# Kernel optimization log

Hardware: AMD Instinct MI355X
Metric: run time of the kernel (lower is better)

The kernel has to match this reference:

```python
import jax, jax.numpy as jnp
import numpy as np
from jax.ops import segment_sum

N_NODES = 50000


def gcn_conv(x, src, dst, W, b, n_nodes):
    # PyG GCNConv with default add_self_loops=True, normalize=True.
    # deg includes self-loops (weight 1 each).
    deg = segment_sum(jnp.ones_like(dst, dtype=x.dtype), dst, num_segments=n_nodes) + 1.0
    dinv = jax.lax.rsqrt(deg)  # [N]
    h = x @ W                  # [N, out]
    # messages over real edges: norm[src]*norm[dst]*h[src]
    msg = h[src] * (dinv[src] * dinv[dst])[:, None]   # [E, out]
    agg = segment_sum(msg, dst, num_segments=n_nodes)  # [N, out]
    # self-loop contribution: dinv[i]^2 * h[i]
    agg = agg + h * (dinv * dinv)[:, None]
    return agg + b


def setup_inputs() -> dict:
    key = jax.random.key(0)
    k1, k2, k3, k4 = jax.random.split(key, 4)
    N, E, d_in, d_hid, d_out = N_NODES, 800000, 128, 128, 64
    x = jax.random.normal(k1, (N, d_in), dtype=jnp.float32)
    edge_index = jax.random.randint(k2, (2, E), 0, N, dtype=jnp.int64)
    W1 = jax.random.normal(k3, (d_in, d_hid), dtype=jnp.float32) / np.sqrt(d_in)
    b1 = jnp.zeros((d_hid,), dtype=jnp.float32)
    W2 = jax.random.normal(k4, (d_hid, d_out), dtype=jnp.float32) / np.sqrt(d_hid)
    b2 = jnp.zeros((d_out,), dtype=jnp.float32)
    return {"x": x, "edge_index": edge_index, "W1": W1, "b1": b1, "W2": W2, "b2": b2}


def reference(x, edge_index, W1, b1, W2, b2):
    src, dst = edge_index[0], edge_index[1]
    h = gcn_conv(x, src, dst, W1, b1, N_NODES)
    h = jax.nn.relu(h)
    out = gcn_conv(h, src, dst, W2, b2, N_NODES)
    return out
```

## Files before the change

### kernel.cpp

```cpp
#include <hip/hip_runtime.h>
#include <hip/hip_bf16.h>


#define ELL_CAP 64
#define NPART 8

typedef __attribute__((ext_vector_type(8))) short short8;
typedef __attribute__((ext_vector_type(4))) float f32x4;

static __device__ __forceinline__ unsigned short f2bf(float f) {
    unsigned int u = __float_as_uint(f);
    u = (u + 0x7fff + ((u >> 16) & 1)) >> 16;
    return (unsigned short)u;
}
static __device__ __forceinline__ float2 bfunpack(unsigned int u) {
    return make_float2(__uint_as_float(u << 16),
                       __uint_as_float(u & 0xffff0000u));
}


__global__ void zero_cnt(int* __restrict__ cnt, int n) {
    int i = blockIdx.x * blockDim.x + threadIdx.x;
    if (i < n) cnt[i] = 0;
}

__global__ __launch_bounds__(256) void build_ell_part(
    const int* __restrict__ src, const int* __restrict__ dst,
    int* __restrict__ cnt, int* __restrict__ ell, int E, int partSize)
{
    const int part   = blockIdx.x & (NPART - 1);
    const int chunk  = blockIdx.x >> 3;
    const int nchunk = gridDim.x >> 3;
    const int lo = part * partSize, hi = lo + partSize;
    const int per = (E + nchunk - 1) / nchunk;
    const int e1 = min((chunk + 1) * per, E);
    for (int e = chunk * per + threadIdx.x; e < e1; e += 256) {
        int d = dst[e];
        if (d >= lo && d < hi) {
            int pos = atomicAdd(&cnt[d], 1);
            if (pos < ELL_CAP) ell[(size_t)d * ELL_CAP + pos] = src[e];
        }
    }
}

__global__ void convert_weights(const float* __restrict__ W1, const float* __restrict__ W2,
                                short* __restrict__ w1t, short* __restrict__ w2t)
{
    int i = blockIdx.x * blockDim.x + threadIdx.x;
    if (i < 128 * 128) {
        int k = i >> 7, nn = i & 127;
        w1t[nn * 128 + k] = (short)f2bf(W1[i]);
    } else if (i < 128 * 128 + 128 * 64) {
        int j = i - 128 * 128;
        int k = j >> 6, nn = j & 63;
        w2t[nn * 128 + k] = (short)f2bf(W2[j]);
    }
}


template<int NC, bool AF32>
__global__ __launch_bounds__(256) void gemm_mfma(
    const void* __restrict__ Av, const short* __restrict__ Bt,
    const int* __restrict__ cnt, unsigned short* __restrict__ Cb, int n)
{
    __shared__ short Bs[NC][136];
    const int tid = threadIdx.x;

    #pragma unroll
    for (int i = 0; i < NC / 16; ++i) {
        int idx = tid + i * 256;
        int nrow = idx >> 4;
        int kcol = (idx & 15) * 8;
        *(short8*)&Bs[nrow][kcol] = *(const short8*)(Bt + nrow * 128 + kcol);
    }
    __syncthreads();

    const int wave = tid >> 6, lane = tid & 63;
    const int row0 = blockIdx.x * 64 + wave * 16;
    if (row0 >= n) return;
    const int quad = lane >> 4, l16 = lane & 15;

    short8 af[4];
    if (AF32) {
        const float* arow = (const float*)Av + (size_t)(row0 + l16) * 128 + quad * 8;
        #pragma unroll
        for (int kk = 0; kk < 4; ++kk) {
            float4 u = *(const float4*)(arow + kk * 32);
            float4 v = *(const float4*)(arow + kk * 32 + 4);
            short8 f;
            f[0] = (short)f2bf(u.x); f[1] = (short)f2bf(u.y);
            f[2] = (short)f2bf(u.z); f[3] = (short)f2bf(u.w);
            f[4] = (short)f2bf(v.x); f[5] = (short)f2bf(v.y);
            f[6] = (short)f2bf(v.z); f[7] = (short)f2bf(v.w);
            af[kk] = f;
        }
    } else {
        const short* arow = (const short*)Av + (size_t)(row0 + l16) * 128 + quad * 8;
        #pragma unroll
        for (int kk = 0; kk < 4; ++kk)
            af[kk] = *(const short8*)(arow + kk * 32);
    }

    float dv[4];
    #pragma unroll
    for (int r = 0; r < 4; ++r)
        dv[r] = rsqrtf((float)cnt[row0 + quad * 4 + r] + 1.0f);

    #pragma unroll
    for (int t = 0; t < NC / 16; ++t) {
        f32x4 acc = {0.f, 0.f, 0.f, 0.f};
        #pragma unroll
        for (int kk = 0; kk < 4; ++kk) {
            short8 bfr = *(const short8*)&Bs[t * 16 + l16][kk * 32 + quad * 8];
            acc = __builtin_amdgcn_mfma_f32_16x16x32_bf16(af[kk], bfr, acc, 0, 0, 0);
        }
        #pragma unroll
        for (int r = 0; r < 4; ++r) {
            int gr = row0 + quad * 4 + r;
            Cb[(size_t)gr * NC + t * 16 + l16] = f2bf(acc[r] * dv[r]);
        }
    }
}


__global__ __launch_bounds__(256) void aggregate_l1(
    const unsigned int* __restrict__ hp, const int* __restrict__ ell,
    const int* __restrict__ cnt, const float* __restrict__ bias,
    unsigned int* __restrict__ z1b, int n)
{
    int node = blockIdx.x * 4 + (threadIdx.x >> 6);
    if (node >= n) return;
    int lane = threadIdx.x & 63;
    int deg = cnt[node];
    float d = rsqrtf((float)deg + 1.0f);
    if (deg > ELL_CAP) deg = ELL_CAP;
    const int* __restrict__ row = ell + (size_t)node * ELL_CAP;

    float2 acc = bfunpack(hp[(size_t)node * 64 + lane]);
    int e = 0;
    for (; e + 4 <= deg; e += 4) {
        int s0 = row[e], s1 = row[e + 1], s2 = row[e + 2], s3 = row[e + 3];
        float2 v0 = bfunpack(hp[(size_t)s0 * 64 + lane]);
        float2 v1 = bfunpack(hp[(size_t)s1 * 64 + lane]);
        float2 v2 = bfunpack(hp[(size_t)s2 * 64 + lane]);
        float2 v3 = bfunpack(hp[(size_t)s3 * 64 + lane]);
        acc.x += (v0.x + v1.x) + (v2.x + v3.x);
        acc.y += (v0.y + v1.y) + (v2.y + v3.y);
    }
    for (; e < deg; ++e) {
        float2 v = bfunpack(hp[(size_t)row[e] * 64 + lane]);
        acc.x += v.x; acc.y += v.y;
    }
    float ox = fmaxf(fmaf(acc.x, d, bias[lane * 2]), 0.f);
    float oy = fmaxf(fmaf(acc.y, d, bias[lane * 2 + 1]), 0.f);
    z1b[(size_t)node * 64 + lane] =
        (unsigned int)f2bf(ox) | ((unsigned int)f2bf(oy) << 16);
}


__global__ __launch_bounds__(256) void aggregate_l2(
    const unsigned int* __restrict__ hp, const int* __restrict__ ell,
    const int* __restrict__ cnt, const float* __restrict__ bias,
    float* __restrict__ out, int n)
{
    int lane = threadIdx.x & 63;
    int half = lane >> 5, l32 = lane & 31;
    int node = blockIdx.x * 8 + (threadIdx.x >> 6) * 2 + half;
    if (node >= n) return;
    int deg = cnt[node];
    float d = rsqrtf((float)deg + 1.0f);
    if (deg > ELL_CAP) deg = ELL_CAP;
    const int* __restrict__ row = ell + (size_t)node * ELL_CAP;

    float2 acc = bfunpack(hp[(size_t)node * 32 + l32]);
    int e = 0;
    for (; e + 4 <= deg; e += 4) {
        int s0 = row[e], s1 = row[e + 1], s2 = row[e + 2], s3 = row[e + 3];
        float2 v0 = bfunpack(hp[(size_t)s0 * 32 + l32]);
        float2 v1 = bfunpack(hp[(size_t)s1 * 32 + l32]);
        float2 v2 = bfunpack(hp[(size_t)s2 * 32 + l32]);
        float2 v3 = bfunpack(hp[(size_t)s3 * 32 + l32]);
        acc.x += (v0.x + v1.x) + (v2.x + v3.x);
        acc.y += (v0.y + v1.y) + (v2.y + v3.y);
    }
    for (; e < deg; ++e) {
        float2 v = bfunpack(hp[(size_t)row[e] * 32 + l32]);
        acc.x += v.x; acc.y += v.y;
    }
    float2 o;
    o.x = fmaf(acc.x, d, bias[l32 * 2]);
    o.y = fmaf(acc.y, d, bias[l32 * 2 + 1]);
    ((float2*)out)[(size_t)node * 32 + l32] = o;
}


extern "C" void kernel_launch(void* const* d_in, const int* in_sizes, int n_in,
                              void* d_out, int out_size, void* d_ws, size_t ws_size,
                              hipStream_t stream)
{
    const float* x  = (const float*)d_in[0];
    const int*   ei = (const int*)d_in[1];
    const float* W1 = (const float*)d_in[2];
    const float* b1 = (const float*)d_in[3];
    const float* W2 = (const float*)d_in[4];
    const float* b2 = (const float*)d_in[5];
    float* out = (float*)d_out;

    const int N = in_sizes[0] / 128;
    const int E = in_sizes[1] / 2;
    const int* src = ei;
    const int* dst = ei + E;
    const int partSize = (N + NPART - 1) / NPART;

    char* ws = (char*)d_ws;
    size_t off = 0;
    auto alloc = [&](size_t bytes) -> void* {
        void* p = ws + off;
        off += (bytes + 255) & ~(size_t)255;
        return p;
    };
    int*            cnt  = (int*)           alloc((size_t)N * 4);
    int*            ell  = (int*)           alloc((size_t)N * ELL_CAP * 4);
    short*          w1t  = (short*)         alloc((size_t)128 * 128 * 2);
    short*          w2t  = (short*)         alloc((size_t)64 * 128 * 2);
    unsigned short* h1b  = (unsigned short*)alloc((size_t)N * 128 * 2);
    unsigned int*   z1b  = (unsigned int*)  alloc((size_t)N * 64 * 4);
    unsigned short* h2b  = (unsigned short*)alloc((size_t)N * 64 * 2);

    convert_weights<<<(128 * 192 + 255) / 256, 256, 0, stream>>>(W1, W2, w1t, w2t);
    zero_cnt<<<(N + 255) / 256, 256, 0, stream>>>(cnt, N);
    build_ell_part<<<128 * NPART, 256, 0, stream>>>(src, dst, cnt, ell, E, partSize);

    gemm_mfma<128, true><<<(N + 63) / 64, 256, 0, stream>>>(x, w1t, cnt, h1b, N);
    aggregate_l1<<<(N + 3) / 4, 256, 0, stream>>>((const unsigned int*)h1b, ell, cnt, b1, z1b, N);

    gemm_mfma<64, false><<<(N + 63) / 64, 256, 0, stream>>>(z1b, w2t, cnt, h2b, N);
    aggregate_l2<<<(N + 7) / 8, 256, 0, stream>>>((const unsigned int*)h2b, ell, cnt, b2, out, N);
}
```

Baseline: 197.3 us.

## Fuse GCN pipeline into one cooperative kernel and overlap ELL build with GEMM1

Replaces the seven-launch pipeline with a single cooperative persistent kernel that uses grid.sync between phases, plus a multi-kernel fallback path. The ELL build now runs concurrently with the first GEMM, which is possible because the dinv[src] scaling moves out of the GEMM and into the layer-1 aggregation as a per-neighbour rsqrt of the count. ELL indices shrink to 16-bit, and the dst-partitioned build is replaced by a single pass over the edges. The aim is to remove launch gaps and overlap the atomic-heavy build with the MFMA work, at the cost of extra count loads per edge and grid-wide barriers on a fixed 768-block grid.

```diff
diff --git a/kernel.cpp b/kernel.cpp
--- a/kernel.cpp
+++ b/kernel.cpp
@@ -1,9 +1,14 @@
 #include <hip/hip_runtime.h>
 #include <hip/hip_bf16.h>
+#include <hip/hip_cooperative_groups.h>
+
+namespace cg = cooperative_groups;
 
 
 #define ELL_CAP 64
-#define NPART 8
+#define COOP_GRID 768
+#define COOP_BUILD 192
+#define FB_BUILD 1024
 
 typedef __attribute__((ext_vector_type(8))) short short8;
 typedef __attribute__((ext_vector_type(4))) float f32x4;
@@ -18,159 +23,148 @@
                        __uint_as_float(u & 0xffff0000u));
 }
 
-
-__global__ void zero_cnt(int* __restrict__ cnt, int n) {
-    int i = blockIdx.x * blockDim.x + threadIdx.x;
-    if (i < n) cnt[i] = 0;
-}
-
-__global__ __launch_bounds__(256) void build_ell_part(
+static __device__ __forceinline__ void build_edges(
     const int* __restrict__ src, const int* __restrict__ dst,
-    int* __restrict__ cnt, int* __restrict__ ell, int E, int partSize)
-{
-    const int part   = blockIdx.x & (NPART - 1);
-    const int chunk  = blockIdx.x >> 3;
-    const int nchunk = gridDim.x >> 3;
-    const int lo = part * partSize, hi = lo + partSize;
-    const int per = (E + nchunk - 1) / nchunk;
-    const int e1 = min((chunk + 1) * per, E);
-    for (int e = chunk * per + threadIdx.x; e < e1; e += 256) {
-        int d = dst[e];
-        if (d >= lo && d < hi) {
-            int pos = atomicAdd(&cnt[d], 1);
-            if (pos < ELL_CAP) ell[(size_t)d * ELL_CAP + pos] = src[e];
+    int* __restrict__ cnt, unsigned short* __restrict__ ell,
+    int E, int start, int stride)
+{
+    for (int e0 = start; e0 < E; e0 += 4 * stride) {
+        #pragma unroll
+        for (int k = 0; k < 4; ++k) {
+            int e = e0 + k * stride;
+            if (e < E) {
+                int d = dst[e];
+                int pos = atomicAdd(&cnt[d], 1);
+                if (pos < ELL_CAP)
+                    ell[(size_t)d * ELL_CAP + pos] = (unsigned short)src[e];
+            }
         }
     }
 }
 
-__global__ void convert_weights(const float* __restrict__ W1, const float* __restrict__ W2,
-                                short* __restrict__ w1t, short* __restrict__ w2t)
-{
-    int i = blockIdx.x * blockDim.x + threadIdx.x;
-    if (i < 128 * 128) {
-        int k = i >> 7, nn = i & 127;
-        w1t[nn * 128 + k] = (short)f2bf(W1[i]);
-    } else if (i < 128 * 128 + 128 * 64) {
-        int j = i - 128 * 128;
-        int k = j >> 6, nn = j & 63;
-        w2t[nn * 128 + k] = (short)f2bf(W2[j]);
-    }
-}
-
-
-template<int NC, bool AF32>
-__global__ __launch_bounds__(256) void gemm_mfma(
-    const void* __restrict__ Av, const short* __restrict__ Bt,
-    const int* __restrict__ cnt, unsigned short* __restrict__ Cb, int n)
-{
-    __shared__ short Bs[NC][136];
+
+template<int NC, bool AF32, bool SCALE>
+static __device__ __forceinline__ void gemm_body(
+    short (*Bs)[136], const void* __restrict__ Av, const short* __restrict__ Bt,
+    const int* __restrict__ cnt, unsigned short* __restrict__ Cb,
+    int n, int bid)
+{
     const int tid = threadIdx.x;
-
-    #pragma unroll
-    for (int i = 0; i < NC / 16; ++i) {
-        int idx = tid + i * 256;
-        int nrow = idx >> 4;
-        int kcol = (idx & 15) * 8;
-        *(short8*)&Bs[nrow][kcol] = *(const short8*)(Bt + nrow * 128 + kcol);
-    }
-    __syncthreads();
-
     const int wave = tid >> 6, lane = tid & 63;
-    const int row0 = blockIdx.x * 64 + wave * 16;
-    if (row0 >= n) return;
+    const int row0 = bid * 64 + wave * 16;
+    const bool active = row0 < n;
     const int quad = lane >> 4, l16 = lane & 15;
 
     short8 af[4];
-    if (AF32) {
-        const float* arow = (const float*)Av + (size_t)(row0 + l16) * 128 + quad * 8;
-        #pragma unroll
-        for (int kk = 0; kk < 4; ++kk) {
-            float4 u = *(const float4*)(arow + kk * 32);
-            float4 v = *(const float4*)(arow + kk * 32 + 4);
-            short8 f;
-            f[0] = (short)f2bf(u.x); f[1] = (short)f2bf(u.y);
-            f[2] = (short)f2bf(u.z); f[3] = (short)f2bf(u.w);
-            f[4] = (short)f2bf(v.x); f[5] = (short)f2bf(v.y);
-            f[6] = (short)f2bf(v.z); f[7] = (short)f2bf(v.w);
-            af[kk] = f;
-        }
-    } else {
-        const short* arow = (const short*)Av + (size_t)(row0 + l16) * 128 + quad * 8;
-        #pragma unroll
-        for (int kk = 0; kk < 4; ++kk)
-            af[kk] = *(const short8*)(arow + kk * 32);
-    }
-
     float dv[4];
-    #pragma unroll
-    for (int r = 0; r < 4; ++r)
-        dv[r] = rsqrtf((float)cnt[row0 + quad * 4 + r] + 1.0f);
-
-    #pragma unroll
-    for (int t = 0; t < NC / 16; ++t) {
-        f32x4 acc = {0.f, 0.f, 0.f, 0.f};
-        #pragma unroll
-        for (int kk = 0; kk < 4; ++kk) {
-            short8 bfr = *(const short8*)&Bs[t * 16 + l16][kk * 32 + quad * 8];
-            acc = __builtin_amdgcn_mfma_f32_16x16x32_bf16(af[kk], bfr, acc, 0, 0, 0);
+    if (active) {
+        if (AF32) {
+            const float* arow = (const float*)Av + (size_t)(row0 + l16) * 128 + quad * 8;
+            #pragma unroll
+            for (int kk = 0; kk < 4; ++kk) {
+                float4 u = *(const float4*)(arow + kk * 32);
+                float4 v = *(const float4*)(arow + kk * 32 + 4);
+                short8 f;
+                f[0] = (short)f2bf(u.x); f[1] = (short)f2bf(u.y);
+                f[2] = (short)f2bf(u.z); f[3] = (short)f2bf(u.w);
+                f[4] = (short)f2bf(v.x); f[5] = (short)f2bf(v.y);
+                f[6] = (short)f2bf(v.z); f[7] = (short)f2bf(v.w);
+                af[kk] = f;
+            }
+        } else {
+            const short* arow = (const short*)Av + (size_t)(row0 + l16) * 128 + quad * 8;
+            #pragma unroll
+            for (int kk = 0; kk < 4; ++kk)
+                af[kk] = *(const short8*)(arow + kk * 32);
         }
         #pragma unroll
-        for (int r = 0; r < 4; ++r) {
-            int gr = row0 + quad * 4 + r;
-            Cb[(size_t)gr * NC + t * 16 + l16] = f2bf(acc[r] * dv[r]);
+        for (int r = 0; r < 4; ++r)
+            dv[r] = SCALE ? rsqrtf((float)cnt[row0 + quad * 4 + r] + 1.0f) : 1.0f;
+    }
+
+    #pragma unroll
+    for (int half = 0; half < NC / 64; ++half) {
+        __syncthreads();
+        #pragma unroll
+        for (int i = 0; i < 4; ++i) {
+            int idx = tid + i * 256;
+            int nrow = idx >> 4;
+            int kcol = (idx & 15) * 8;
+            *(short8*)&Bs[nrow][kcol] =
+                *(const short8*)(Bt + (size_t)(half * 64 + nrow) * 128 + kcol);
         }
-    }
-}
-
-
-__global__ __launch_bounds__(256) void aggregate_l1(
-    const unsigned int* __restrict__ hp, const int* __restrict__ ell,
-    const int* __restrict__ cnt, const float* __restrict__ bias,
-    unsigned int* __restrict__ z1b, int n)
-{
-    int node = blockIdx.x * 4 + (threadIdx.x >> 6);
-    if (node >= n) return;
-    int lane = threadIdx.x & 63;
-    int deg = cnt[node];
-    float d = rsqrtf((float)deg + 1.0f);
-    if (deg > ELL_CAP) deg = ELL_CAP;
-    const int* __restrict__ row = ell + (size_t)node * ELL_CAP;
-
-    float2 acc = bfunpack(hp[(size_t)node * 64 + lane]);
+        __syncthreads();
+        if (active) {
+            #pragma unroll
+            for (int t = 0; t < 4; ++t) {
+                f32x4 acc = {0.f, 0.f, 0.f, 0.f};
+                #pragma unroll
+                for (int kk = 0; kk < 4; ++kk) {
+                    short8 bfr = *(const short8*)&Bs[t * 16 + l16][kk * 32 + quad * 8];
+                    acc = __builtin_amdgcn_mfma_f32_16x16x32_bf16(af[kk], bfr, acc, 0, 0, 0);
+                }
+                #pragma unroll
+                for (int r = 0; r < 4; ++r) {
+                    int gr = row0 + quad * 4 + r;
+                    Cb[(size_t)gr * NC + half * 64 + t * 16 + l16] =
+                        f2bf(SCALE ? acc[r] * dv[r] : acc[r]);
+                }
+            }
+        }
+    }
+    __syncthreads();
+}
+
+
+static __device__ __forceinline__ void agg1_node(
+    int node, int lane, const unsigned int* __restrict__ hp,
+    const unsigned short* __restrict__ ell, const int* __restrict__ cnt,
+    const float* __restrict__ bias, unsigned int* __restrict__ z1b)
+{
+    int rawdeg = cnt[node];
+    float dn = rsqrtf((float)rawdeg + 1.0f);
+    int deg = min(rawdeg, ELL_CAP);
+    const unsigned short* __restrict__ row = ell + (size_t)node * ELL_CAP;
+
+    float2 self = bfunpack(hp[(size_t)node * 64 + lane]);
+    float2 acc = make_float2(self.x * dn, self.y * dn);
     int e = 0;
     for (; e + 4 <= deg; e += 4) {
         int s0 = row[e], s1 = row[e + 1], s2 = row[e + 2], s3 = row[e + 3];
+        float d0 = rsqrtf((float)cnt[s0] + 1.0f);
+        float d1 = rsqrtf((float)cnt[s1] + 1.0f);
+        float d2 = rsqrtf((float)cnt[s2] + 1.0f);
+        float d3 = rsqrtf((float)cnt[s3] + 1.0f);
         float2 v0 = bfunpack(hp[(size_t)s0 * 64 + lane]);
         float2 v1 = bfunpack(hp[(size_t)s1 * 64 + lane]);
         float2 v2 = bfunpack(hp[(size_t)s2 * 64 + lane]);
         float2 v3 = bfunpack(hp[(size_t)s3 * 64 + lane]);
-        acc.x += (v0.x + v1.x) + (v2.x + v3.x);
-        acc.y += (v0.y + v1.y) + (v2.y + v3.y);
+        acc.x = fmaf(v0.x, d0, fmaf(v1.x, d1, fmaf(v2.x, d2, fmaf(v3.x, d3, acc.x))));
+        acc.y = fmaf(v0.y, d0, fmaf(v1.y, d1, fmaf(v2.y, d2, fmaf(v3.y, d3, acc.y))));
     }
     for (; e < deg; ++e) {
-        float2 v = bfunpack(hp[(size_t)row[e] * 64 + lane]);
-        acc.x += v.x; acc.y += v.y;
-    }
-    float ox = fmaxf(fmaf(acc.x, d, bias[lane * 2]), 0.f);
-    float oy = fmaxf(fmaf(acc.y, d, bias[lane * 2 + 1]), 0.f);
+        int s = row[e];
+        float ds = rsqrtf((float)cnt[s] + 1.0f);
+        float2 v = bfunpack(hp[(size_t)s * 64 + lane]);
+        acc.x = fmaf(v.x, ds, acc.x);
+        acc.y = fmaf(v.y, ds, acc.y);
+    }
+    float ox = fmaxf(fmaf(acc.x, dn, bias[lane * 2]), 0.f);
+    float oy = fmaxf(fmaf(acc.y, dn, bias[lane * 2 + 1]), 0.f);
     z1b[(size_t)node * 64 + lane] =
         (unsigned int)f2bf(ox) | ((unsigned int)f2bf(oy) << 16);
 }
 
 
-__global__ __launch_bounds__(256) void aggregate_l2(
-    const unsigned int* __restrict__ hp, const int* __restrict__ ell,
-    const int* __restrict__ cnt, const float* __restrict__ bias,
-    float* __restrict__ out, int n)
-{
-    int lane = threadIdx.x & 63;
-    int half = lane >> 5, l32 = lane & 31;
-    int node = blockIdx.x * 8 + (threadIdx.x >> 6) * 2 + half;
-    if (node >= n) return;
-    int deg = cnt[node];
-    float d = rsqrtf((float)deg + 1.0f);
-    if (deg > ELL_CAP) deg = ELL_CAP;
-    const int* __restrict__ row = ell + (size_t)node * ELL_CAP;
+static __device__ __forceinline__ void agg2_node(
+    int node, int l32, const unsigned int* __restrict__ hp,
+    const unsigned short* __restrict__ ell, const int* __restrict__ cnt,
+    const float* __restrict__ bias, float* __restrict__ out)
+{
+    int rawdeg = cnt[node];
+    float dn = rsqrtf((float)rawdeg + 1.0f);
+    int deg = min(rawdeg, ELL_CAP);
+    const unsigned short* __restrict__ row = ell + (size_t)node * ELL_CAP;
 
     float2 acc = bfunpack(hp[(size_t)node * 32 + l32]);
     int e = 0;
@@ -188,9 +182,126 @@
         acc.x += v.x; acc.y += v.y;
     }
     float2 o;
-    o.x = fmaf(acc.x, d, bias[l32 * 2]);
-    o.y = fmaf(acc.y, d, bias[l32 * 2 + 1]);
+    o.x = fmaf(acc.x, dn, bias[l32 * 2]);
+    o.y = fmaf(acc.y, dn, bias[l32 * 2 + 1]);
     ((float2*)out)[(size_t)node * 32 + l32] = o;
+}
+
+
+__global__ __launch_bounds__(256) void gcn_fused(
+    const int* __restrict__ src, const int* __restrict__ dst,
+    const float* __restrict__ x,
+    const float* __restrict__ W1, const float* __restrict__ b1,
+    const float* __restrict__ W2, const float* __restrict__ b2,
+    int* __restrict__ cnt, unsigned short* __restrict__ ell,
+    short* __restrict__ w1t, short* __restrict__ w2t,
+    unsigned short* __restrict__ h1b, unsigned int* __restrict__ z1b,
+    unsigned short* __restrict__ h2b, float* __restrict__ out,
+    int N, int E)
+{
+    __shared__ short Bs[64][136];
+    cg::grid_group grid = cg::this_grid();
+    const int tid = threadIdx.x;
+    const int bid = blockIdx.x;
+    const int gsize = gridDim.x;
+    const int gthreads = gsize * 256;
+    const int gtid = bid * 256 + tid;
+    const int wave = tid >> 6, lane = tid & 63;
+    const int ntiles = (N + 63) / 64;
+
+    for (int i = gtid; i < N; i += gthreads) cnt[i] = 0;
+    for (int i = gtid; i < 128 * 128; i += gthreads) {
+        int k = i >> 7, nn = i & 127;
+        w1t[nn * 128 + k] = (short)f2bf(W1[i]);
+    }
+    for (int i = gtid; i < 128 * 64; i += gthreads) {
+        int k = i >> 6, nn = i & 63;
+        w2t[nn * 128 + k] = (short)f2bf(W2[i]);
+    }
+    grid.sync();
+
+    if (bid < COOP_BUILD) {
+        build_edges(src, dst, cnt, ell, E, bid * 256 + tid, COOP_BUILD * 256);
+    } else {
+        for (int t = bid - COOP_BUILD; t < ntiles; t += gsize - COOP_BUILD)
+            gemm_body<128, true, false>(Bs, x, w1t, nullptr, h1b, N, t);
+    }
+    grid.sync();
+
+    for (int node = bid * 4 + wave; node < N; node += gsize * 4)
+        agg1_node(node, lane, (const unsigned int*)h1b, ell, cnt, b1, z1b);
+    grid.sync();
+
+    for (int t = bid; t < ntiles; t += gsize)
+        gemm_body<64, false, true>(Bs, z1b, w2t, cnt, h2b, N, t);
+    grid.sync();
+
+    {
+        const int half = lane >> 5, l32 = lane & 31;
+        for (int node = bid * 8 + wave * 2 + half; node < N; node += gsize * 8)
+            agg2_node(node, l32, (const unsigned int*)h2b, ell, cnt, b2, out);
+    }
+}
+
+
+__global__ __launch_bounds__(256) void prep_k(
+    const float* __restrict__ W1, const float* __restrict__ W2,
+    short* __restrict__ w1t, short* __restrict__ w2t,
+    int* __restrict__ cnt, int N)
+{
+    int i = blockIdx.x * blockDim.x + threadIdx.x;
+    if (i < N) cnt[i] = 0;
+    if (i < 128 * 128) {
+        int k = i >> 7, nn = i & 127;
+        w1t[nn * 128 + k] = (short)f2bf(W1[i]);
+    } else if (i < 128 * 128 + 128 * 64) {
+        int j = i - 128 * 128;
+        int k = j >> 6, nn = j & 63;
+        w2t[nn * 128 + k] = (short)f2bf(W2[j]);
+    }
+}
+
+__global__ __launch_bounds__(256) void build_gemm1_k(
+    const int* __restrict__ src, const int* __restrict__ dst,
+    int* __restrict__ cnt, unsigned short* __restrict__ ell, int E, int n,
+    const float* __restrict__ x, const short* __restrict__ w1t,
+    unsigned short* __restrict__ h1b)
+{
+    __shared__ short Bs[64][136];
+    if (blockIdx.x < FB_BUILD) {
+        build_edges(src, dst, cnt, ell, E,
+                    blockIdx.x * 256 + threadIdx.x, FB_BUILD * 256);
+    } else {
+        gemm_body<128, true, false>(Bs, x, w1t, nullptr, h1b, n,
+                                    blockIdx.x - FB_BUILD);
+    }
+}
+
+__global__ __launch_bounds__(256) void agg1_k(
+    const unsigned int* __restrict__ hp, const unsigned short* __restrict__ ell,
+    const int* __restrict__ cnt, const float* __restrict__ bias,
+    unsigned int* __restrict__ z1b, int n)
+{
+    int node = blockIdx.x * 4 + (threadIdx.x >> 6);
+    if (node < n) agg1_node(node, threadIdx.x & 63, hp, ell, cnt, bias, z1b);
+}
+
+__global__ __launch_bounds__(256) void gemm2_k(
+    const unsigned int* __restrict__ z1b, const short* __restrict__ w2t,
+    const int* __restrict__ cnt, unsigned short* __restrict__ h2b, int n)
+{
+    __shared__ short Bs[64][136];
+    gemm_body<64, false, true>(Bs, z1b, w2t, cnt, h2b, n, blockIdx.x);
+}
+
+__global__ __launch_bounds__(256) void agg2_k(
+    const unsigned int* __restrict__ hp, const unsigned short* __restrict__ ell,
+    const int* __restrict__ cnt, const float* __restrict__ bias,
+    float* __restrict__ out, int n)
+{
+    int lane = threadIdx.x & 63;
+    int node = blockIdx.x * 8 + (threadIdx.x >> 6) * 2 + (lane >> 5);
+    if (node < n) agg2_node(node, lane & 31, hp, ell, cnt, bias, out);
 }
 
 
@@ -206,11 +317,10 @@
     const float* b2 = (const float*)d_in[5];
     float* out = (float*)d_out;
 
-    const int N = in_sizes[0] / 128;
-    const int E = in_sizes[1] / 2;
+    int N = in_sizes[0] / 128;
+    int E = in_sizes[1] / 2;
     const int* src = ei;
     const int* dst = ei + E;
-    const int partSize = (N + NPART - 1) / NPART;
 
     char* ws = (char*)d_ws;
     size_t off = 0;
@@ -219,21 +329,34 @@
         off += (bytes + 255) & ~(size_t)255;
         return p;
     };
-    int*            cnt  = (int*)           alloc((size_t)N * 4);
-    int*            ell  = (int*)           alloc((size_t)N * ELL_CAP * 4);
-    short*          w1t  = (short*)         alloc((size_t)128 * 128 * 2);
-    short*          w2t  = (short*)         alloc((size_t)64 * 128 * 2);
-    unsigned short* h1b  = (unsigned short*)alloc((size_t)N * 128 * 2);
-    unsigned int*   z1b  = (unsigned int*)  alloc((size_t)N * 64 * 4);
-    unsigned short* h2b  = (unsigned short*)alloc((size_t)N * 64 * 2);
-
-    convert_weights<<<(128 * 192 + 255) / 256, 256, 0, stream>>>(W1, W2, w1t, w2t);
-    zero_cnt<<<(N + 255) / 256, 256, 0, stream>>>(cnt, N);
-    build_ell_part<<<128 * NPART, 256, 0, stream>>>(src, dst, cnt, ell, E, partSize);
-
-    gemm_mfma<128, true><<<(N + 63) / 64, 256, 0, stream>>>(x, w1t, cnt, h1b, N);
-    aggregate_l1<<<(N + 3) / 4, 256, 0, stream>>>((const unsigned int*)h1b, ell, cnt, b1, z1b, N);
-
-    gemm_mfma<64, false><<<(N + 63) / 64, 256, 0, stream>>>(z1b, w2t, cnt, h2b, N);
-    aggregate_l2<<<(N + 7) / 8, 256, 0, stream>>>((const unsigned int*)h2b, ell, cnt, b2, out, N);
-}
+    int*            cnt = (int*)           alloc((size_t)N * 4);
+    unsigned short* ell = (unsigned short*)alloc((size_t)N * ELL_CAP * 2);
+    short*          w1t = (short*)         alloc((size_t)128 * 128 * 2);
+    short*          w2t = (short*)         alloc((size_t)64 * 128 * 2);
+    unsigned short* h1b = (unsigned short*)alloc((size_t)N * 128 * 2);
+    unsigned int*   z1b = (unsigned int*)  alloc((size_t)N * 64 * 4);
+    unsigned short* h2b = (unsigned short*)alloc((size_t)N * 64 * 2);
+
+    void* args[] = {
+        (void*)&src, (void*)&dst, (void*)&x,
+        (void*)&W1, (void*)&b1, (void*)&W2, (void*)&b2,
+        (void*)&cnt, (void*)&ell, (void*)&w1t, (void*)&w2t,
+        (void*)&h1b, (void*)&z1b, (void*)&h2b, (void*)&out,
+        (void*)&N, (void*)&E
+    };
+    hipError_t err = hipLaunchCooperativeKernel((const void*)gcn_fused,
+                                                dim3(COOP_GRID), dim3(256),
+                                                args, 0, stream);
+    if (err != hipSuccess) {
+        const int gemm1Blocks = (N + 63) / 64;
+        prep_k<<<(N + 255) / 256, 256, 0, stream>>>(W1, W2, w1t, w2t, cnt, N);
+        build_gemm1_k<<<FB_BUILD + gemm1Blocks, 256, 0, stream>>>(
+            src, dst, cnt, ell, E, N, x, w1t, h1b);
+        agg1_k<<<(N + 3) / 4, 256, 0, stream>>>(
+            (const unsigned int*)h1b, ell, cnt, b1, z1b, N);
+        gemm2_k<<<gemm1Blocks, 256, 0, stream>>>(
+            (const unsigned int*)z1b, w2t, cnt, h2b, N);
+        agg2_k<<<(N + 7) / 8, 256, 0, stream>>>(
+            (const unsigned int*)h2b, ell, cnt, b2, out, N);
+    }
+}
```

Result: slower. 579.2 us (+193.6%).
